# Kernel optimization log

Measured on AMD Instinct MI355X. Metric: run time of the kernel, lower is better.

## Reference

```python
import jax, jax.numpy as jnp
import numpy as np

B, S, D, H = 8, 512, 1024, 16
DK = D // H          # 64
N_ASP = 4            # aspect tokens per sample
NEG = -1000000000.0


def setup_inputs() -> dict:
    key = jax.random.key(0)
    ks = jax.random.split(key, 12)
    return {
        "query": jax.random.normal(ks[0], (B, S, D), jnp.float32),
        "key_in": jax.random.normal(ks[1], (B, S, D), jnp.float32),
        "mask": jax.random.randint(ks[2], (B, S, S), 0, 2).astype(jnp.int32),
        "aspect": jax.random.normal(ks[3], (B, 1, D), jnp.float32),
        "aspect_ids": jax.random.randint(ks[4], (B, N_ASP), 0, S),
        # learned params
        "Wq": jax.random.normal(ks[5], (D, D), jnp.float32) / np.sqrt(D).astype(np.float32),
        "bq": jnp.zeros((D,), jnp.float32),
        "Wk": jax.random.normal(ks[6], (D, D), jnp.float32) / np.sqrt(D).astype(np.float32),
        "bk": jnp.zeros((D,), jnp.float32),
        "Wd": jax.random.normal(ks[7], (D, DK), jnp.float32) / np.sqrt(D).astype(np.float32),
        "bd": jnp.zeros((DK,), jnp.float32),
        "weight_m": jax.random.normal(ks[8], (H, DK, DK), jnp.float32) / np.sqrt(DK).astype(np.float32),
        "bias_m": jnp.zeros((1,), jnp.float32),
    }


def reference(query, key_in, mask, aspect, aspect_ids,
              Wq, bq, Wk, bk, Wd, bd, weight_m, bias_m):
    # projections -> [B,H,S,DK]
    q = (query @ Wq + bq).reshape(B, S, H, DK).transpose(0, 2, 1, 3)
    k = (key_in @ Wk + bk).reshape(B, S, H, DK).transpose(0, 2, 1, 3)

    # aspect -> dense -> broadcast to [B,H,S,DK]
    asp = aspect @ Wd + bd                                  # [B,1,DK]
    asp = jnp.broadcast_to(asp[:, None, :, :], (B, H, S, DK))

    # asps = tanh(aspect @ W_m @ K^T + bias_m)  -> [B,H,S,S]
    aw = jnp.einsum('bhsd,hde->bhse', asp, weight_m)
    asps = jnp.tanh(jnp.einsum('bhse,bhte->bhst', aw, k) + bias_m[0])

    # per-(batch,head) average score vector over rows -> [B,H,S]
    avg = asps.sum(axis=-2) / S

    # scatter: for each aspect index, overwrite its row and column with avg
    # (sequential over the small fixed N_ASP, matching torch write order:
    #  row write then column write per index)
    a_sc = asps
    bidx = jnp.arange(B)
    for j in range(N_ASP):
        idx = aspect_ids[:, j]                              # [B]
        a_sc = a_sc.at[bidx, :, idx, :].set(avg)            # rows
        a_sc = a_sc.at[bidx, :, :, idx].set(avg)            # cols

    # standard masked attention probs
    scores = jnp.einsum('bhsd,bhtd->bhst', q, k) / np.float32(np.sqrt(DK))
    scores = jnp.where(mask[:, None, :, :] == 0, NEG, scores)
    attn = jax.nn.softmax(scores, axis=-1)
    return a_sc, attn
```

## Files before the change

kernel.cpp:

```cpp
#include <hip/hip_runtime.h>

typedef __bf16 bf16x8 __attribute__((ext_vector_type(8)));
typedef float  f32x4  __attribute__((ext_vector_type(4)));

__device__ __forceinline__ unsigned short f2bf(float f) {
  union { float f; unsigned u; } x; x.f = f;
  unsigned r = (x.u + 0x7FFFu + ((x.u >> 16) & 1u)) >> 16;
  return (unsigned short)r;
}

__device__ __forceinline__ void gload_lds16(const void* g, void* l) {
  __builtin_amdgcn_global_load_lds((__attribute__((address_space(1))) void*)g,
                                   (__attribute__((address_space(3))) void*)l,
                                   16, 0, 0);
}

__global__ __launch_bounds__(256)
void prep_fused_kernel(const float* __restrict__ query, const float* __restrict__ key_in,
                       const float* __restrict__ Wq, const float* __restrict__ Wk,
                       const float* __restrict__ aspect, const float* __restrict__ Wd,
                       const float* __restrict__ bd, const float* __restrict__ weight_m,
                       const float* __restrict__ bk, const int* __restrict__ mask,
                       unsigned short* __restrict__ Aq, unsigned short* __restrict__ Ak,
                       unsigned short* __restrict__ Wqt, unsigned short* __restrict__ Wkt,
                       float* __restrict__ u_out, float* __restrict__ c_out,
                       unsigned long long* __restrict__ mb) {
  __shared__ __align__(16) char smem[2112];
  const int bx = blockIdx.x, tid = threadIdx.x;
  if (bx >= 2560) {
    int i = (bx - 2560) * 256 + tid;
    if (i < 1048576) {
      float4 x = ((const float4*)query)[i];
      ushort4 y; y.x = f2bf(x.x); y.y = f2bf(x.y); y.z = f2bf(x.z); y.w = f2bf(x.w);
      ((ushort4*)Aq)[i] = y;
    } else {
      int j = i - 1048576;
      float4 x = ((const float4*)key_in)[j];
      ushort4 y; y.x = f2bf(x.x); y.y = f2bf(x.y); y.z = f2bf(x.z); y.w = f2bf(x.w);
      ((ushort4*)Ak)[j] = y;
    }
  } else if (bx >= 512) {
    int t = bx - 512;
    const float* W = (t >> 10) ? Wk : Wq;
    unsigned short* Wt = (t >> 10) ? Wkt : Wqt;
    int tile_id = t & 1023;
    int k0 = (tile_id & 31) * 32, n0 = (tile_id >> 5) * 32;
    int tx = tid & 31, ty = tid >> 5;
    unsigned short (*tile)[33] = (unsigned short (*)[33])smem;
    #pragma unroll
    for (int i = 0; i < 4; ++i) {
      int k = ty + i * 8;
      tile[k][tx] = f2bf(W[(size_t)(k0 + k) * 1024 + n0 + tx]);
    }
    __syncthreads();
    #pragma unroll
    for (int i = 0; i < 4; ++i) {
      int n = ty + i * 8;
      Wt[(size_t)(n0 + n) * 1024 + k0 + tx] = tile[tx][n];
    }
  } else if (bx >= 256) {
    int t = bx - 256;
    int gw = (t * 256 + tid) >> 6, lane = tid & 63;
    for (int row = gw; row < 4096; row += 1024) {
      const int* mr = mask + (size_t)row * 512;
      unsigned long long* dst = mb + (size_t)row * 8;
      #pragma unroll
      for (int it = 0; it < 8; ++it) {
        int m = mr[it * 64 + lane];
        unsigned long long bb = __ballot(m != 0);
        if (lane == 0) dst[it] = bb;
      }
    }
  } else {
    int id = bx;
    int bh = id >> 1, b = bh >> 4, h = bh & 15;
    int dbase = (id & 1) * 512;
    int e = tid & 63, g = tid >> 6;
    float* part  = (float*)smem;
    float* asp_s = part + 256;
    float* aw_s  = asp_s + 64;
    const float* arow = aspect + (size_t)b * 1024;
    float acc = 0.f;
    for (int d = g * 256; d < g * 256 + 256; ++d)
      acc += arow[d] * Wd[(size_t)d * 64 + e];
    part[g * 64 + e] = acc;
    __syncthreads();
    if (tid < 64)
      asp_s[tid] = bd[tid] + part[tid] + part[64 + tid] + part[128 + tid] + part[192 + tid];
    __syncthreads();
    if (tid < 64) {
      const float* wm = weight_m + (size_t)h * 4096;
      float aw = 0.f;
      #pragma unroll 8
      for (int d = 0; d < 64; ++d) aw += asp_s[d] * wm[d * 64 + tid];
      aw_s[tid] = aw;
    }
    __syncthreads();
    float awl = aw_s[e];
    if ((id & 1) == 0 && g == 0) {
      float s = bk[h * 64 + e] * awl;
      #pragma unroll
      for (int off = 32; off >= 1; off >>= 1) s += __shfl_xor(s, off, 64);
      if (e == 0) c_out[bh] = s;
    }
    const float* wkcol = Wk + h * 64 + e;
    #pragma unroll 2
    for (int it = 0; it < 32; ++it) {
      int d0 = dbase + g * 128 + it * 4;
      float s0 = wkcol[(size_t)d0 * 1024] * awl;
      float s1 = wkcol[(size_t)(d0 + 1) * 1024] * awl;
      float s2 = wkcol[(size_t)(d0 + 2) * 1024] * awl;
      float s3 = wkcol[(size_t)(d0 + 3) * 1024] * awl;
      #pragma unroll
      for (int off = 32; off >= 1; off >>= 1) {
        s0 += __shfl_xor(s0, off, 64);
        s1 += __shfl_xor(s1, off, 64);
        s2 += __shfl_xor(s2, off, 64);
        s3 += __shfl_xor(s3, off, 64);
      }
      if (e == 0) {
        float4 uo = {s0, s1, s2, s3};
        *(float4*)(u_out + (size_t)bh * 1024 + d0) = uo;
      }
    }
  }
}

__global__ __launch_bounds__(256, 2)
void gemm_v_kernel(const unsigned short* __restrict__ Aq, const unsigned short* __restrict__ Ak,
                   const unsigned short* __restrict__ Bq, const unsigned short* __restrict__ Bk,
                   const float* __restrict__ bq, const float* __restrict__ bk,
                   unsigned short* __restrict__ qb, unsigned short* __restrict__ kb,
                   const float* __restrict__ key_in, const float* __restrict__ u,
                   const float* __restrict__ c, const float* __restrict__ bias_m,
                   float* __restrict__ v) {
  __shared__ __align__(16) char smem[32768];
  const int bx = blockIdx.x, tid = threadIdx.x;
  if (bx < 512) {
    const int z = bx >> 8;
    const unsigned short* A  = z ? Ak : Aq;
    const unsigned short* Bt = z ? Bk : Bq;
    const float* bias = z ? bk : bq;
    unsigned short* out = z ? kb : qb;
    const int m0 = (bx & 31) * 128, n0 = ((bx >> 5) & 7) * 128;
    unsigned short* As = (unsigned short*)smem;
    unsigned short* Bs = (unsigned short*)(smem + 16384);
    const int wid = tid >> 6, lane = tid & 63;
    const int wr = wid >> 1, wc = wid & 1;
    const int quad = lane >> 4, l15 = lane & 15;
    const int srw = lane >> 3;
    const int jcol = ((lane & 7) ^ srw) * 8;
    const int p0 = (quad ^ (l15 & 7)) * 8;
    f32x4 acc[4][4] = {};
    for (int k0 = 0; k0 < 1024; k0 += 64) {
      #pragma unroll
      for (int i = 0; i < 4; ++i) {
        int r = wid * 32 + i * 8 + srw;
        gload_lds16(A  + (size_t)(m0 + r) * 1024 + k0 + jcol, As + (wid * 32 + i * 8) * 64);
        gload_lds16(Bt + (size_t)(n0 + r) * 1024 + k0 + jcol, Bs + (wid * 32 + i * 8) * 64);
      }
      __syncthreads();
      bf16x8 af[4][2], bfr[4][2];
      #pragma unroll
      for (int mi = 0; mi < 4; ++mi) {
        const unsigned short* base = As + (wr * 64 + mi * 16 + l15) * 64;
        af[mi][0] = *(const bf16x8*)(base + p0);
        af[mi][1] = *(const bf16x8*)(base + (p0 ^ 32));
      }
      #pragma unroll
      for (int ni = 0; ni < 4; ++ni) {
        const unsigned short* base = Bs + (wc * 64 + ni * 16 + l15) * 64;
        bfr[ni][0] = *(const bf16x8*)(base + p0);
        bfr[ni][1] = *(const bf16x8*)(base + (p0 ^ 32));
      }
      #pragma unroll
      for (int mi = 0; mi < 4; ++mi)
        #pragma unroll
        for (int ni = 0; ni < 4; ++ni) {
          acc[mi][ni] = __builtin_amdgcn_mfma_f32_16x16x32_bf16(af[mi][0], bfr[ni][0], acc[mi][ni], 0, 0, 0);
          acc[mi][ni] = __builtin_amdgcn_mfma_f32_16x16x32_bf16(af[mi][1], bfr[ni][1], acc[mi][ni], 0, 0, 0);
        }
      __syncthreads();
    }
    #pragma unroll
    for (int mi = 0; mi < 4; ++mi) {
      #pragma unroll
      for (int ni = 0; ni < 4; ++ni) {
        const int n = n0 + wc * 64 + ni * 16 + l15;
        const int hh = n >> 6, dk = n & 63;
        const float bv = bias[n];
        #pragma unroll
        for (int r = 0; r < 4; ++r) {
          const int m = m0 + wr * 64 + mi * 16 + quad * 4 + r;
          const int bb = m >> 9, ss = m & 511;
          out[(((size_t)bb * 16 + hh) * 512 + ss) * 64 + dk] = f2bf(acc[mi][ni][r] + bv);
        }
      }
    }
  } else {
    int vb = bx - 512;
    int b = vb >> 6, t0 = (vb & 63) * 8;
    int wid = tid >> 6, lane = tid & 63;
    float (*ks_)[1024] = (float (*)[1024])smem;
    const float4* ksrc = (const float4*)(key_in + ((size_t)b * 512 + t0) * 1024);
    float4* kdst = (float4*)&ks_[0][0];
    for (int i = tid; i < 2048; i += 256) kdst[i] = ksrc[i];
    __syncthreads();
    const float* ub = u + (size_t)b * 16384;
    int r0 = wid * 2;
    float acc0[16] = {}, acc1[16] = {};
    for (int i = 0; i < 16; ++i) {
      int col = lane + 64 * i;
      float kv0 = ks_[r0][col], kv1 = ks_[r0 + 1][col];
      #pragma unroll
      for (int h = 0; h < 16; ++h) {
        float uv = ub[h * 1024 + col];
        acc0[h] += kv0 * uv;
        acc1[h] += kv1 * uv;
      }
    }
    float cb = bias_m[0];
    #pragma unroll
    for (int h = 0; h < 16; ++h) {
      float a0 = acc0[h], a1 = acc1[h];
      #pragma unroll
      for (int off = 32; off >= 1; off >>= 1) {
        a0 += __shfl_xor(a0, off, 64);
        a1 += __shfl_xor(a1, off, 64);
      }
      if (lane == h) {
        int bh = b * 16 + h;
        float cc = c[bh] + cb;
        v[(size_t)bh * 512 + t0 + r0]     = tanhf(a0 + cc);
        v[(size_t)bh * 512 + t0 + r0 + 1] = tanhf(a1 + cc);
      }
    }
  }
}

__global__ __launch_bounds__(256, 2)
void attn_asc_kernel(const unsigned short* __restrict__ qb, const unsigned short* __restrict__ kb,
                     const unsigned* __restrict__ mbits, const float* __restrict__ vv,
                     const int* __restrict__ ids, float* __restrict__ attn,
                     float* __restrict__ out_asc) {
  const int bx = blockIdx.x, tid = threadIdx.x;
  if (bx < 1024) {
    const int bh = bx & 127, b = bh >> 4;
    const int s0 = (bx >> 7) * 64;
    const int wid = tid >> 6, lane = tid & 63;
    const int quad = lane >> 4, l15 = lane & 15;
    const unsigned short* kslab = kb + (size_t)bh * 512 * 64;
    const unsigned short* qslab = qb + ((size_t)bh * 512 + s0) * 64;
    const unsigned short* qptr = qslab + (wid * 16 + l15) * 64 + quad * 8;
    bf16x8 af0 = *(const bf16x8*)(qptr);
    bf16x8 af1 = *(const bf16x8*)(qptr + 32);
    const unsigned short* kptr = kslab + l15 * 64 + quad * 8;
    f32x4 acc[32];
    #pragma unroll
    for (int tile = 0; tile < 32; ++tile) {
      bf16x8 b0 = *(const bf16x8*)(kptr + tile * 1024);
      bf16x8 b1 = *(const bf16x8*)(kptr + tile * 1024 + 32);
      f32x4 a = {0.f, 0.f, 0.f, 0.f};
      a = __builtin_amdgcn_mfma_f32_16x16x32_bf16(af0, b0, a, 0, 0, 0);
      a = __builtin_amdgcn_mfma_f32_16x16x32_bf16(af1, b1, a, 0, 0, 0);
      acc[tile] = a;
    }
    const size_t srow = (size_t)s0 + wid * 16 + quad * 4;
    const unsigned* mrow = mbits + ((size_t)b * 512 + srow) * 16;
    float mx[4] = {-3.0e38f, -3.0e38f, -3.0e38f, -3.0e38f};
    #pragma unroll
    for (int tp = 0; tp < 16; ++tp) {
      #pragma unroll
      for (int r = 0; r < 4; ++r) {
        unsigned m = mrow[(size_t)r * 16 + tp];
        float sc0 = acc[2 * tp][r] * 0.125f;
        float sc1 = acc[2 * tp + 1][r] * 0.125f;
        sc0 = ((m >> l15) & 1u) ? sc0 : -1.0e9f;
        sc1 = ((m >> (16 + l15)) & 1u) ? sc1 : -1.0e9f;
        acc[2 * tp][r] = sc0;
        acc[2 * tp + 1][r] = sc1;
        mx[r] = fmaxf(mx[r], fmaxf(sc0, sc1));
      }
    }
    #pragma unroll
    for (int r = 0; r < 4; ++r)
      #pragma unroll
      for (int off = 1; off < 16; off <<= 1)
        mx[r] = fmaxf(mx[r], __shfl_xor(mx[r], off, 64));
    float sm[4] = {0.f, 0.f, 0.f, 0.f};
    #pragma unroll
    for (int tile = 0; tile < 32; ++tile)
      #pragma unroll
      for (int r = 0; r < 4; ++r) {
        float e = __expf(acc[tile][r] - mx[r]);
        acc[tile][r] = e;
        sm[r] += e;
      }
    #pragma unroll
    for (int r = 0; r < 4; ++r) {
      #pragma unroll
      for (int off = 1; off < 16; off <<= 1)
        sm[r] += __shfl_xor(sm[r], off, 64);
      sm[r] = 1.0f / sm[r];
    }
    float* obase = attn + ((size_t)bh * 512 + srow) * 512 + l15;
    #pragma unroll
    for (int r = 0; r < 4; ++r)
      #pragma unroll
      for (int tile = 0; tile < 32; ++tile)
        __builtin_nontemporal_store(acc[tile][r] * sm[r], &obase[(size_t)r * 512 + tile * 16]);
  } else {
    size_t i4 = (size_t)(bx - 1024) * 256 + tid;
    int t0 = (int)(i4 & 127) * 4;
    int s  = (int)(i4 >> 7) & 511;
    int bh = (int)(i4 >> 16);
    int b  = bh >> 4;
    int i0 = ids[b * 4], i1 = ids[b * 4 + 1], i2 = ids[b * 4 + 2], i3 = ids[b * 4 + 3];
    #define LASTOF(t) ((i3==(t))?3:(i2==(t))?2:(i1==(t))?1:(i0==(t))?0:-1)
    int ls  = LASTOF(s);
    int lt0 = LASTOF(t0), lt1 = LASTOF(t0+1), lt2 = LASTOF(t0+2), lt3 = LASTOF(t0+3);
    #undef LASTOF
    const float* vrow = vv + (size_t)bh * 512;
    float vs = vrow[s];
    float4 vt = *(const float4*)(vrow + t0);
    f32x4 o;
    o[0] = (lt0 >= 0 && lt0 >= ls) ? vs : vt.x;
    o[1] = (lt1 >= 0 && lt1 >= ls) ? vs : vt.y;
    o[2] = (lt2 >= 0 && lt2 >= ls) ? vs : vt.z;
    o[3] = (lt3 >= 0 && lt3 >= ls) ? vs : vt.w;
    __builtin_nontemporal_store(o, ((f32x4*)out_asc) + i4);
  }
}

extern "C" void kernel_launch(void* const* d_in, const int* in_sizes, int n_in,
                              void* d_out, int out_size, void* d_ws, size_t ws_size,
                              hipStream_t stream) {
  const float* query    = (const float*)d_in[0];
  const float* key_in   = (const float*)d_in[1];
  const int*   mask     = (const int*)d_in[2];
  const float* aspect   = (const float*)d_in[3];
  const int*   a_ids    = (const int*)d_in[4];
  const float* Wq       = (const float*)d_in[5];
  const float* bq       = (const float*)d_in[6];
  const float* Wk       = (const float*)d_in[7];
  const float* bk       = (const float*)d_in[8];
  const float* Wd       = (const float*)d_in[9];
  const float* bd       = (const float*)d_in[10];
  const float* weight_m = (const float*)d_in[11];
  const float* bias_m   = (const float*)d_in[12];

  float* out_asc  = (float*)d_out;
  float* out_attn = out_asc + 33554432ull;

  char* ws = (char*)d_ws;
  unsigned short* Aq   = (unsigned short*)(ws);
  unsigned short* Ak   = (unsigned short*)(ws + 8388608);
  unsigned short* Wqt  = (unsigned short*)(ws + 16777216);
  unsigned short* Wkt  = (unsigned short*)(ws + 18874368);
  unsigned short* qbuf = (unsigned short*)(ws + 20971520);
  unsigned short* kbuf = (unsigned short*)(ws + 29360128);
  float* u   = (float*)(ws + 37748736);
  float* c   = (float*)(ws + 38273024);
  float* v   = (float*)(ws + 38277120);
  unsigned long long* mb = (unsigned long long*)(ws + 38539264);

  prep_fused_kernel<<<dim3(10752), dim3(256), 0, stream>>>(
      query, key_in, Wq, Wk, aspect, Wd, bd, weight_m, bk, mask,
      Aq, Ak, Wqt, Wkt, u, c, mb);
  gemm_v_kernel<<<dim3(1024), dim3(256), 0, stream>>>(
      Aq, Ak, Wqt, Wkt, bq, bk, qbuf, kbuf, key_in, u, c, bias_m, v);
  attn_asc_kernel<<<dim3(33792), dim3(256), 0, stream>>>(
      qbuf, kbuf, (const unsigned*)mb, v, a_ids, out_attn, out_asc);
}
```

Measured before the change: 431.1 us.

## Stage Q and K tiles through swizzled LDS with direct global-to-LDS loads

The attention kernel now copies the Q block and K slab into shared memory with global_load_lds, using an XOR swizzle to avoid bank conflicts. MFMA operands then come from LDS instead of strided per-lane global loads. K is loaded in two halves of 256 rows with barriers in between. This aims to coalesce global traffic, but it adds barriers, serializes the two K halves, and uses about 40KB of LDS, which may limit occupancy.

```diff
diff --git a/kernel.cpp b/kernel.cpp
--- a/kernel.cpp
+++ b/kernel.cpp
@@ -243,23 +243,50 @@
                      const unsigned* __restrict__ mbits, const float* __restrict__ vv,
                      const int* __restrict__ ids, float* __restrict__ attn,
                      float* __restrict__ out_asc) {
+  __shared__ __align__(16) unsigned short ks[256 * 64];
+  __shared__ __align__(16) unsigned short qs[64 * 64];
   const int bx = blockIdx.x, tid = threadIdx.x;
   if (bx < 1024) {
     const int bh = bx & 127, b = bh >> 4;
     const int s0 = (bx >> 7) * 64;
     const int wid = tid >> 6, lane = tid & 63;
     const int quad = lane >> 4, l15 = lane & 15;
+    const int srw = lane >> 3;
+    const int j8 = ((lane & 7) ^ srw) * 8;
+    const int p0 = (quad ^ (l15 & 7)) * 8;
     const unsigned short* kslab = kb + (size_t)bh * 512 * 64;
     const unsigned short* qslab = qb + ((size_t)bh * 512 + s0) * 64;
-    const unsigned short* qptr = qslab + (wid * 16 + l15) * 64 + quad * 8;
-    bf16x8 af0 = *(const bf16x8*)(qptr);
-    bf16x8 af1 = *(const bf16x8*)(qptr + 32);
-    const unsigned short* kptr = kslab + l15 * 64 + quad * 8;
+    #pragma unroll
+    for (int i = 0; i < 2; ++i)
+      gload_lds16(qslab + (wid * 2 + i) * 512 + srw * 64 + j8, qs + (wid * 2 + i) * 512);
+    #pragma unroll
+    for (int i = 0; i < 8; ++i)
+      gload_lds16(kslab + (wid * 8 + i) * 512 + srw * 64 + j8, ks + (wid * 8 + i) * 512);
+    __syncthreads();
+    const unsigned short* qbase = qs + (wid * 16 + l15) * 64;
+    bf16x8 af0 = *(const bf16x8*)(qbase + p0);
+    bf16x8 af1 = *(const bf16x8*)(qbase + (p0 ^ 32));
     f32x4 acc[32];
     #pragma unroll
-    for (int tile = 0; tile < 32; ++tile) {
-      bf16x8 b0 = *(const bf16x8*)(kptr + tile * 1024);
-      bf16x8 b1 = *(const bf16x8*)(kptr + tile * 1024 + 32);
+    for (int tile = 0; tile < 16; ++tile) {
+      const unsigned short* kbase = ks + (tile * 16 + l15) * 64;
+      bf16x8 b0 = *(const bf16x8*)(kbase + p0);
+      bf16x8 b1 = *(const bf16x8*)(kbase + (p0 ^ 32));
+      f32x4 a = {0.f, 0.f, 0.f, 0.f};
+      a = __builtin_amdgcn_mfma_f32_16x16x32_bf16(af0, b0, a, 0, 0, 0);
+      a = __builtin_amdgcn_mfma_f32_16x16x32_bf16(af1, b1, a, 0, 0, 0);
+      acc[tile] = a;
+    }
+    __syncthreads();
+    #pragma unroll
+    for (int i = 0; i < 8; ++i)
+      gload_lds16(kslab + 16384 + (wid * 8 + i) * 512 + srw * 64 + j8, ks + (wid * 8 + i) * 512);
+    __syncthreads();
+    #pragma unroll
+    for (int tile = 16; tile < 32; ++tile) {
+      const unsigned short* kbase = ks + ((tile - 16) * 16 + l15) * 64;
+      bf16x8 b0 = *(const bf16x8*)(kbase + p0);
+      bf16x8 b1 = *(const bf16x8*)(kbase + (p0 ^ 32));
       f32x4 a = {0.f, 0.f, 0.f, 0.f};
       a = __builtin_amdgcn_mfma_f32_16x16x32_bf16(af0, b0, a, 0, 0, 0);
       a = __builtin_amdgcn_mfma_f32_16x16x32_bf16(af1, b1, a, 0, 0, 0);
```

New measurement: 409.5 us. -5.0%, faster.
